# Optimization experiments

Measured on AMD Instinct MI355X. Metric: run time of the kernel, lower is better.

## Reference

```python
import jax, jax.numpy as jnp
import numpy as np

HID = 51

def _lstm_cell_zero_state(x, w_ih, w_hh, b_ih, b_hh):
    # torch LSTMCell with h=c=0: gates = x @ W_ih^T + b_ih + b_hh (W_hh term vanishes)
    gates = x @ w_ih.T + (b_ih + b_hh)
    i, f, g, o = jnp.split(gates, 4, axis=-1)
    i = jax.nn.sigmoid(i)
    g = jnp.tanh(g)
    o = jax.nn.sigmoid(o)
    c = i * g  # f * c_prev = 0
    h = o * jnp.tanh(c)
    return h


def setup_inputs() -> dict:
    key = jax.random.key(0)
    ks = jax.random.split(key, 12)
    T, B = 200, 2048
    s1 = 1.0  # torch default init is U(-1/sqrt(hid), 1/sqrt(hid))
    bound = 1.0 / np.sqrt(HID)
    u = lambda k, shp: jax.random.uniform(k, shp, jnp.float32, -bound, bound)
    return {
        "x": jax.random.normal(ks[0], (T, B, 1), jnp.float32),
        "w_ih1": u(ks[1], (4 * HID, 1)),
        "w_hh1": u(ks[2], (4 * HID, HID)),
        "b_ih1": u(ks[3], (4 * HID,)),
        "b_hh1": u(ks[4], (4 * HID,)),
        "w_ih2": u(ks[5], (4 * HID, HID)),
        "w_hh2": u(ks[6], (4 * HID, HID)),
        "b_ih2": u(ks[7], (4 * HID,)),
        "b_hh2": u(ks[8], (4 * HID,)),
        "w_lin": u(ks[9], (1, HID)),
        "b_lin": u(ks[10], (1,)),
    }


def reference(x, w_ih1, w_hh1, b_ih1, b_hh1, w_ih2, w_hh2, b_ih2, b_hh2, w_lin, b_lin):
    # Original never carries (h, c) between timesteps -> every timestep is an
    # independent zero-state cell application; vectorize over (T, B) at once.
    T, B, D = x.shape
    xf = x.reshape(T * B, D)
    h1 = _lstm_cell_zero_state(xf, w_ih1, w_hh1, b_ih1, b_hh1)   # [T*B, 51]
    h2 = _lstm_cell_zero_state(h1, w_ih2, w_hh2, b_ih2, b_hh2)   # [T*B, 51]
    out = h2 @ w_lin.T + b_lin                                    # [T*B, 1]
    return out.reshape(T, B, 1)
```

## Files before the change

### kernel.cpp

```cpp
#include <hip/hip_runtime.h>
#include <math.h>


#define NTAB 16384
#define XMIN (-10.0f)
#define XMAX (10.0f)

typedef _Float16 h2_t __attribute__((ext_vector_type(2)));

__device__ __forceinline__ float fexp2_(float x) { return __builtin_amdgcn_exp2f(x); }
__device__ __forceinline__ float frcp_(float x)  { return __builtin_amdgcn_rcpf(x); }
__device__ __forceinline__ float fsig_(float z)  { return frcp_(1.0f + fexp2_(-1.44269504f * z)); }
__device__ __forceinline__ float ftanh_(float z) { return 1.0f - 2.0f * frcp_(1.0f + fexp2_(2.88539008f * z)); }

__global__ __launch_bounds__(256) void repack(
    const float* __restrict__ w_ih2, const float* __restrict__ b_ih2,
    const float* __restrict__ b_hh2, unsigned int* __restrict__ Wp,
    float* __restrict__ B2)
{
    int g = blockIdx.x * 256 + threadIdx.x;
    if (g < 153 * 26) {
        int r = g / 26;
        int p = g - r * 26;
        int src = (r < 51) ? r : r + 51;
        float a = w_ih2[src * 51 + 2 * p];
        float b = (2 * p + 1 < 51) ? w_ih2[src * 51 + 2 * p + 1] : 0.0f;
        h2_t h;
        h.x = (_Float16)a;
        h.y = (_Float16)b;
        Wp[r * 26 + p] = __builtin_bit_cast(unsigned int, h);
    }
    if (g < 153) {
        int src = (g < 51) ? g : g + 51;
        B2[g] = b_ih2[src] + b_hh2[src];
    }
}

__global__ __launch_bounds__(1024, 4) void build_table(
    const float* __restrict__ w_ih1, const float* __restrict__ b_ih1, const float* __restrict__ b_hh1,
    const unsigned int* __restrict__ Wp, const float* __restrict__ B2,
    const float* __restrict__ w_lin, const float* __restrict__ b_lin,
    float* __restrict__ table)
{
    __shared__ float h1s[51][64];
    __shared__ float sPart[16][64];

    const int tid  = threadIdx.x;
    const int lane = tid & 63;
    const int wave = __builtin_amdgcn_readfirstlane(tid >> 6);

    const int   e = blockIdx.x * 64 + lane;
    const float x = XMIN + (XMAX - XMIN) * ((float)e / (float)(NTAB - 1));

    for (int j = wave; j < 51; j += 16) {
        float gi = fmaf(x, w_ih1[j],       b_ih1[j]       + b_hh1[j]);
        float gg = fmaf(x, w_ih1[j + 102], b_ih1[j + 102] + b_hh1[j + 102]);
        float go = fmaf(x, w_ih1[j + 153], b_ih1[j + 153] + b_hh1[j + 153]);
        float c  = fsig_(gi) * ftanh_(gg);
        h1s[j][lane] = fsig_(go) * ftanh_(c);
    }
    __syncthreads();

    h2_t h1p[26];
    #pragma unroll
    for (int p = 0; p < 26; ++p) {
        float a = h1s[2 * p][lane];
        float b = (2 * p + 1 < 51) ? h1s[2 * p + 1][lane] : 0.0f;
        h2_t h;
        h.x = (_Float16)a;
        h.y = (_Float16)b;
        h1p[p] = h;
    }

    float part = 0.0f;
    for (int j = wave; j < 51; j += 16) {
        const unsigned int* __restrict__ Wi = Wp + j * 26;
        const unsigned int* __restrict__ Wg = Wp + (51 + j) * 26;
        const unsigned int* __restrict__ Wo = Wp + (102 + j) * 26;
        float gi = B2[j];
        float gg = B2[51 + j];
        float go = B2[102 + j];
        #pragma unroll
        for (int p = 0; p < 26; ++p) {
            gi = __builtin_amdgcn_fdot2(h1p[p], __builtin_bit_cast(h2_t, Wi[p]), gi, false);
            gg = __builtin_amdgcn_fdot2(h1p[p], __builtin_bit_cast(h2_t, Wg[p]), gg, false);
            go = __builtin_amdgcn_fdot2(h1p[p], __builtin_bit_cast(h2_t, Wo[p]), go, false);
        }
        float c2  = fsig_(gi) * ftanh_(gg);
        float h2v = fsig_(go) * ftanh_(c2);
        part = fmaf(h2v, w_lin[j], part);
    }

    sPart[wave][lane] = part;
    __syncthreads();
    if (wave == 0) {
        float out = b_lin[0];
        #pragma unroll
        for (int w = 0; w < 16; ++w) out += sPart[w][lane];
        table[e] = out;
    }
}

__device__ __forceinline__ float lerp_tab(float x, const float* __restrict__ t) {
    const float inv_h = (float)(NTAB - 1) / (XMAX - XMIN);
    float u = (x - XMIN) * inv_h;
    u = fminf(fmaxf(u, 0.0f), (float)(NTAB - 1) - 0.001f);
    int   i0 = (int)u;
    float f  = u - (float)i0;
    float t0 = t[i0];
    float t1 = t[i0 + 1];
    return fmaf(f, t1 - t0, t0);
}

__global__ __launch_bounds__(256) void lookup_kernel(
    const float* __restrict__ x, const float* __restrict__ table,
    float* __restrict__ out, int n)
{
    int i4 = blockIdx.x * 256 + threadIdx.x;
    int base = i4 * 4;
    if (base + 3 < n) {
        float4 xv = ((const float4*)x)[i4];
        float4 r;
        r.x = lerp_tab(xv.x, table);
        r.y = lerp_tab(xv.y, table);
        r.z = lerp_tab(xv.z, table);
        r.w = lerp_tab(xv.w, table);
        ((float4*)out)[i4] = r;
    } else {
        for (int i = base; i < n; ++i) out[i] = lerp_tab(x[i], table);
    }
}

extern "C" void kernel_launch(void* const* d_in, const int* in_sizes, int n_in,
                              void* d_out, int out_size, void* d_ws, size_t ws_size,
                              hipStream_t stream) {
    const float* x     = (const float*)d_in[0];
    const float* w_ih1 = (const float*)d_in[1];
    const float* b_ih1 = (const float*)d_in[3];
    const float* b_hh1 = (const float*)d_in[4];
    const float* w_ih2 = (const float*)d_in[5];
    const float* b_ih2 = (const float*)d_in[7];
    const float* b_hh2 = (const float*)d_in[8];
    const float* w_lin = (const float*)d_in[9];
    const float* b_lin = (const float*)d_in[10];

    float* out = (float*)d_out;
    float*        table = (float*)d_ws;
    unsigned int* Wp    = (unsigned int*)d_ws + 16384;
    float*        B2    = (float*)d_ws + 16384 + 153 * 26;
    const int n = in_sizes[0];

    repack<<<(153 * 26 + 255) / 256, 256, 0, stream>>>(w_ih2, b_ih2, b_hh2, Wp, B2);

    build_table<<<NTAB / 64, 1024, 0, stream>>>(
        w_ih1, b_ih1, b_hh1, Wp, B2, w_lin, b_lin, table);

    const int n4 = (n + 3) / 4;
    lookup_kernel<<<(n4 + 255) / 256, 256, 0, stream>>>(x, table, out, n);
}
```

Measured before the change: 84.31 us.

## Store scratch table and weights in output tail instead of workspace

Places the packed weights, biases and two copies of the lookup table in the last region of the output buffer rather than in the workspace. The main lookup covers everything except that tail region. A two-block tail kernel then copies each table into shared memory and overwrites the tail region with the real results, so no block reads a table copy it is overwriting. The apparent aim is to avoid workspace use or to keep the table cache-resident next to the output. The cost is an extra launch, a serial tail of about 37K elements handled by only two blocks, and a dependency on the output being at least that large.

New measurement: 88.55 us. 5.0% more time.

```diff
diff --git a/kernel.cpp b/kernel.cpp
--- a/kernel.cpp
+++ b/kernel.cpp
@@ -40,7 +40,7 @@
     const float* __restrict__ w_ih1, const float* __restrict__ b_ih1, const float* __restrict__ b_hh1,
     const unsigned int* __restrict__ Wp, const float* __restrict__ B2,
     const float* __restrict__ w_lin, const float* __restrict__ b_lin,
-    float* __restrict__ table)
+    float* __restrict__ tabA, float* __restrict__ tabB)
 {
     __shared__ float h1s[51][64];
     __shared__ float sPart[16][64];
@@ -97,7 +97,8 @@
         float out = b_lin[0];
         #pragma unroll
         for (int w = 0; w < 16; ++w) out += sPart[w][lane];
-        table[e] = out;
+        tabA[e] = out;
+        tabB[e] = out;
     }
 }
 
@@ -112,13 +113,13 @@
     return fmaf(f, t1 - t0, t0);
 }
 
-__global__ __launch_bounds__(256) void lookup_kernel(
+__global__ __launch_bounds__(256) void lookup_main(
     const float* __restrict__ x, const float* __restrict__ table,
-    float* __restrict__ out, int n)
+    float* __restrict__ out, int nlim)
 {
     int i4 = blockIdx.x * 256 + threadIdx.x;
     int base = i4 * 4;
-    if (base + 3 < n) {
+    if (base + 3 < nlim) {
         float4 xv = ((const float4*)x)[i4];
         float4 r;
         r.x = lerp_tab(xv.x, table);
@@ -127,7 +128,31 @@
         r.w = lerp_tab(xv.w, table);
         ((float4*)out)[i4] = r;
     } else {
-        for (int i = base; i < n; ++i) out[i] = lerp_tab(x[i], table);
+        for (int i = base; i < nlim; ++i) out[i] = lerp_tab(x[i], table);
+    }
+}
+
+__global__ __launch_bounds__(1024) void lookup_tail(
+    const float* __restrict__ x, float* __restrict__ out,
+    int wpB, int copy0, int copy1, int n)
+{
+    __shared__ float tab[NTAB];
+    const int b = blockIdx.x;
+    const float* __restrict__ src = out + (b == 0 ? copy1 : copy0);
+    for (int i = threadIdx.x; i < NTAB; i += 1024) tab[i] = src[i];
+    __syncthreads();
+
+    const int begin = (b == 0) ? wpB : copy0;
+    const int end   = (b == 0) ? copy0 : n;
+    const float inv_h = (float)(NTAB - 1) / (XMAX - XMIN);
+    for (int i = begin + (int)threadIdx.x; i < end; i += 1024) {
+        float u = (x[i] - XMIN) * inv_h;
+        u = fminf(fmaxf(u, 0.0f), (float)(NTAB - 1) - 0.001f);
+        int   i0 = (int)u;
+        float f  = u - (float)i0;
+        float t0 = tab[i0];
+        float t1 = tab[i0 + 1];
+        out[i] = fmaf(f, t1 - t0, t0);
     }
 }
 
@@ -145,16 +170,25 @@
     const float* b_lin = (const float*)d_in[10];
 
     float* out = (float*)d_out;
-    float*        table = (float*)d_ws;
-    unsigned int* Wp    = (unsigned int*)d_ws + 16384;
-    float*        B2    = (float*)d_ws + 16384 + 153 * 26;
-    const int n = in_sizes[0];
+    (void)d_ws; (void)ws_size;
+
+    const int n     = in_sizes[0];
+    const int copy0 = n - NTAB;
+    const int copy1 = copy0 - NTAB;
+    const int wpB   = copy1 - 4160;
+
+    unsigned int* Wp   = (unsigned int*)out + wpB;
+    float*        B2   = out + wpB + 4000;
+    float*        tabA = out + copy1;
+    float*        tabB = out + copy0;
 
     repack<<<(153 * 26 + 255) / 256, 256, 0, stream>>>(w_ih2, b_ih2, b_hh2, Wp, B2);
 
     build_table<<<NTAB / 64, 1024, 0, stream>>>(
-        w_ih1, b_ih1, b_hh1, Wp, B2, w_lin, b_lin, table);
+        w_ih1, b_ih1, b_hh1, Wp, B2, w_lin, b_lin, tabA, tabB);
 
-    const int n4 = (n + 3) / 4;
-    lookup_kernel<<<(n4 + 255) / 256, 256, 0, stream>>>(x, table, out, n);
+    const int n4 = wpB / 4;
+    lookup_main<<<(n4 + 255) / 256, 256, 0, stream>>>(x, tabB, out, wpB);
+
+    lookup_tail<<<2, 1024, 0, stream>>>(x, out, wpB, copy0, copy1, n);
 }
```
